# Kernel tuning notes

Hardware: AMD Instinct MI355X
Metric: run time of the kernel (lower is better)

## Reference

```python
import jax, jax.numpy as jnp
import numpy as np

EPS = 1e-6

def _log_g(x):
    # log of continuous g(x) = where(x>=0, x+0.5, sigmoid(x)) from minGRU paper
    return jnp.where(x >= 0, jnp.log(jax.nn.relu(x) + 0.5), -jax.nn.softplus(-x))

def setup_inputs() -> dict:
    key = jax.random.key(0)
    ks = jax.random.split(key, 4)
    B, S, D, E = 4, 2048, 1024, 8
    scale = D ** -0.5
    return {
        "inputs": jax.random.normal(ks[0], (B, S, D), dtype=jnp.float32),
        "norm_weight": jnp.ones((D,), jnp.float32),
        "router_w": jax.random.normal(ks[1], (E, D), jnp.float32) * scale,
        "router_b": jnp.zeros((E,), jnp.float32),
        "w_hg": jax.random.normal(ks[2], (E, 2 * D, D), jnp.float32) * scale,
        "w_out": jax.random.normal(ks[3], (E, D, D), jnp.float32) * scale,
    }

def reference(inputs, norm_weight, router_w, router_b, w_hg, w_out):
    D = inputs.shape[-1]
    # --- RMSNorm ---
    x = inputs * jax.lax.rsqrt(jnp.mean(inputs * inputs, axis=-1, keepdims=True) + EPS) * norm_weight
    # --- SMEAR: per-sample soft merge of expert weights via mean-pooled routing ---
    probs = jax.nn.softmax(jnp.mean(x, axis=1) @ router_w.T + router_b, axis=-1)  # [B,E]
    W_hg = jnp.einsum('be,ekd->bkd', probs, w_hg)    # [B,2D,D] merged to_hidden_and_gate
    W_out = jnp.einsum('be,eod->bod', probs, w_out)  # [B,D,D]  merged to_out
    # --- minGRU with merged weights (log-space parallel scan, no initial state) ---
    hg = jnp.einsum('bsd,bkd->bsk', x, W_hg)         # [B,S,2D]
    hidden, gate = hg[..., :D], hg[..., D:]
    log_coeffs = -jax.nn.softplus(gate)                      # log(1 - z_t)
    log_values = -jax.nn.softplus(-gate) + _log_g(hidden)    # log z_t + log g(h~_t)
    a_star = jnp.cumsum(log_coeffs, axis=1)
    log_h = a_star + jax.lax.cumlogsumexp(log_values - a_star, axis=1)
    h = jnp.exp(log_h)                               # [B,S,D] recurrent states
    new_state = h[:, -1:]                            # [B,1,D]
    out = jnp.einsum('bsk,bok->bso', h, W_out)       # proj_out
    aux_loss = jnp.zeros((), inputs.dtype)
    return (out + inputs, new_state, aux_loss)
```

## Files before the change

### kernel.cpp

```cpp
#include <hip/hip_runtime.h>
#include <hip/hip_bf16.h>
#include <hip/hip_fp16.h>

#define B_  4
#define S_  2048
#define D_  1024
#define E_  8
#define K2_ 2048

#define CHUNKS 64
#define CLEN   32

typedef __attribute__((ext_vector_type(8))) short short8;
typedef __attribute__((ext_vector_type(4))) float floatx4;

__device__ __forceinline__ void gld16(const void* g, const void* l) {
    __builtin_amdgcn_global_load_lds(
        (const __attribute__((address_space(1))) unsigned int*)g,
        (__attribute__((address_space(3))) unsigned int*)l, 16, 0, 0);
}

__device__ __forceinline__ unsigned short f2bf(float f) {
    unsigned int u = __float_as_uint(f);
    u += 0x7fffu + ((u >> 16) & 1u);
    return (unsigned short)(u >> 16);
}

__global__ void rmsnorm_k(const float* __restrict__ in, const float* __restrict__ nw,
                          __hip_bfloat16* __restrict__ x) {
    int b = blockIdx.y, s = blockIdx.x, t = threadIdx.x;
    const float4* row = (const float4*)(in + ((size_t)b * S_ + s) * D_);
    float4 v = row[t];
    float ss = v.x * v.x + v.y * v.y + v.z * v.z + v.w * v.w;
#pragma unroll
    for (int o = 32; o > 0; o >>= 1) ss += __shfl_down(ss, o, 64);
    __shared__ float ls[4];
    if ((t & 63) == 0) ls[t >> 6] = ss;
    __syncthreads();
    float tot = ls[0] + ls[1] + ls[2] + ls[3];
    float rs = rsqrtf(tot * (1.0f / (float)D_) + 1e-6f);
    float4 w = ((const float4*)nw)[t];
    ushort4 o;
    o.x = f2bf(v.x * rs * w.x); o.y = f2bf(v.y * rs * w.y);
    o.z = f2bf(v.z * rs * w.z); o.w = f2bf(v.w * rs * w.w);
    ((ushort4*)(x + ((size_t)b * S_ + s) * D_))[t] = o;
}

__global__ void xsum_k(const __hip_bfloat16* __restrict__ x, float* __restrict__ xs) {
    int d = blockIdx.x * 256 + threadIdx.x;
    int b = blockIdx.y;
    int s0 = blockIdx.z * 128;
    const __hip_bfloat16* p = x + ((size_t)b * S_ + s0) * D_ + d;
    float acc = 0.0f;
#pragma unroll 4
    for (int s = 0; s < 128; s++) { acc += __bfloat162float(*p); p += D_; }
    atomicAdd(&xs[b * D_ + d], acc);
}

__global__ void router_k(const float* __restrict__ xs, const float* __restrict__ rw,
                         const float* __restrict__ rb, float* __restrict__ probs,
                         float* __restrict__ aux) {
    int t = threadIdx.x;
    if (t == 255) *aux = 0.0f;
    int pair = t >> 3, sub = t & 7;
    int b = pair >> 3, e = pair & 7;
    float acc = 0.0f;
#pragma unroll 8
    for (int d = sub; d < D_; d += 8) acc += xs[b * D_ + d] * rw[e * D_ + d];
#pragma unroll
    for (int o = 4; o > 0; o >>= 1) acc += __shfl_down(acc, o, 8);
    __shared__ float lg[32];
    if (sub == 0) lg[pair] = acc * (1.0f / (float)S_) + rb[e];
    __syncthreads();
    if (t < 4) {
        float m = -1e30f;
        for (int e2 = 0; e2 < 8; e2++) m = fmaxf(m, lg[t * 8 + e2]);
        float ssum = 0.0f; float ex[8];
        for (int e2 = 0; e2 < 8; e2++) { ex[e2] = expf(lg[t * 8 + e2] - m); ssum += ex[e2]; }
        for (int e2 = 0; e2 < 8; e2++) probs[t * 8 + e2] = ex[e2] / ssum;
    }
}

__global__ void mix_k(const float* __restrict__ probs, const float* __restrict__ whg_e,
                      const float* __restrict__ wout_e, __hip_bfloat16* __restrict__ Whg,
                      __hip_bfloat16* __restrict__ Wout) {
    __shared__ float P[32];
    int t = threadIdx.x;
    if (t < 32) P[t] = probs[t];
    __syncthreads();
    size_t i4 = (size_t)blockIdx.x * 256 + t;
    const size_t T1q = (size_t)K2_ * D_ / 4;
    const size_t T2q = (size_t)D_ * D_ / 4;
    float4 a0 = {0,0,0,0}, a1 = {0,0,0,0}, a2 = {0,0,0,0}, a3 = {0,0,0,0};
    if (i4 < T1q) {
        const float4* src = (const float4*)whg_e;
#pragma unroll
        for (int e = 0; e < 8; e++) {
            float4 wv = src[(size_t)e * T1q + i4];
            float p0 = P[e], p1 = P[8 + e], p2 = P[16 + e], p3 = P[24 + e];
            a0.x += p0 * wv.x; a0.y += p0 * wv.y; a0.z += p0 * wv.z; a0.w += p0 * wv.w;
            a1.x += p1 * wv.x; a1.y += p1 * wv.y; a1.z += p1 * wv.z; a1.w += p1 * wv.w;
            a2.x += p2 * wv.x; a2.y += p2 * wv.y; a2.z += p2 * wv.z; a2.w += p2 * wv.w;
            a3.x += p3 * wv.x; a3.y += p3 * wv.y; a3.z += p3 * wv.z; a3.w += p3 * wv.w;
        }
        ushort4* dst = (ushort4*)Whg;
        ushort4 o;
        o.x = f2bf(a0.x); o.y = f2bf(a0.y); o.z = f2bf(a0.z); o.w = f2bf(a0.w);
        dst[0 * T1q + i4] = o;
        o.x = f2bf(a1.x); o.y = f2bf(a1.y); o.z = f2bf(a1.z); o.w = f2bf(a1.w);
        dst[1 * T1q + i4] = o;
        o.x = f2bf(a2.x); o.y = f2bf(a2.y); o.z = f2bf(a2.z); o.w = f2bf(a2.w);
        dst[2 * T1q + i4] = o;
        o.x = f2bf(a3.x); o.y = f2bf(a3.y); o.z = f2bf(a3.z); o.w = f2bf(a3.w);
        dst[3 * T1q + i4] = o;
    } else {
        size_t j4 = i4 - T1q;
        const float4* src = (const float4*)wout_e;
#pragma unroll
        for (int e = 0; e < 8; e++) {
            float4 wv = src[(size_t)e * T2q + j4];
            float p0 = P[e], p1 = P[8 + e], p2 = P[16 + e], p3 = P[24 + e];
            a0.x += p0 * wv.x; a0.y += p0 * wv.y; a0.z += p0 * wv.z; a0.w += p0 * wv.w;
            a1.x += p1 * wv.x; a1.y += p1 * wv.y; a1.z += p1 * wv.z; a1.w += p1 * wv.w;
            a2.x += p2 * wv.x; a2.y += p2 * wv.y; a2.z += p2 * wv.z; a2.w += p2 * wv.w;
            a3.x += p3 * wv.x; a3.y += p3 * wv.y; a3.z += p3 * wv.z; a3.w += p3 * wv.w;
        }
        ushort4* dst = (ushort4*)Wout;
        ushort4 o;
        o.x = f2bf(a0.x); o.y = f2bf(a0.y); o.z = f2bf(a0.z); o.w = f2bf(a0.w);
        dst[0 * T2q + j4] = o;
        o.x = f2bf(a1.x); o.y = f2bf(a1.y); o.z = f2bf(a1.z); o.w = f2bf(a1.w);
        dst[1 * T2q + j4] = o;
        o.x = f2bf(a2.x); o.y = f2bf(a2.y); o.z = f2bf(a2.z); o.w = f2bf(a2.w);
        dst[2 * T2q + j4] = o;
        o.x = f2bf(a3.x); o.y = f2bf(a3.y); o.z = f2bf(a3.z); o.w = f2bf(a3.w);
        dst[3 * T2q + j4] = o;
    }
}

__global__ __launch_bounds__(512, 2) void gemm_hg_cv(
    const __hip_bfloat16* __restrict__ A, const __hip_bfloat16* __restrict__ Bm,
    __half2* __restrict__ cv) {
    const int K = D_;
    int bz = blockIdx.z;
    A  += (size_t)bz * S_ * D_;
    Bm += (size_t)bz * K2_ * D_;
    __half2* CV = cv + (size_t)bz * S_ * D_;
    int id = blockIdx.x;
    int sw = (id & 7) * 8 + (id >> 3);
    int m0 = (sw >> 3) * 256, n0 = (sw & 7) * 128;
    __shared__ __hip_bfloat16 lA[2][256][64];
    __shared__ __hip_bfloat16 lBh[2][128][64];
    __shared__ __hip_bfloat16 lBg[2][128][64];
    int t = threadIdx.x;
    int w = t >> 6, lane = t & 63;
    int lm = lane & 15, quad = lane >> 4;
    int wr = w >> 1, wc = w & 1;
    floatx4 acch[4][4] = {};
    floatx4 accg[4][4] = {};
    int srow = lane >> 3;
    int swzb = ((lane & 7) ^ srow) * 16;

    const __hip_bfloat16* Bh = Bm;
    const __hip_bfloat16* Bg = Bm + (size_t)D_ * K;

    const char* pA[4]; const char* pBhp[2]; const char* pBgp[2];
#pragma unroll
    for (int it = 0; it < 4; it++)
        pA[it] = (const char*)(A + (size_t)(m0 + (w * 4 + it) * 8 + srow) * K) + swzb;
#pragma unroll
    for (int it = 0; it < 2; it++) {
        pBhp[it] = (const char*)(Bh + (size_t)(n0 + (w * 2 + it) * 8 + srow) * K) + swzb;
        pBgp[it] = (const char*)(Bg + (size_t)(n0 + (w * 2 + it) * 8 + srow) * K) + swzb;
    }

    auto stage_part = [&](int bb, int part) {
        if (part == 0) {
            gld16(pA[0], &lA[bb][(w * 4 + 0) * 8][0]); pA[0] += 128;
            gld16(pA[1], &lA[bb][(w * 4 + 1) * 8][0]); pA[1] += 128;
            gld16(pBhp[0], &lBh[bb][(w * 2 + 0) * 8][0]); pBhp[0] += 128;
            gld16(pBgp[0], &lBg[bb][(w * 2 + 0) * 8][0]); pBgp[0] += 128;
        } else {
            gld16(pA[2], &lA[bb][(w * 4 + 2) * 8][0]); pA[2] += 128;
            gld16(pA[3], &lA[bb][(w * 4 + 3) * 8][0]); pA[3] += 128;
            gld16(pBhp[1], &lBh[bb][(w * 2 + 1) * 8][0]); pBhp[1] += 128;
            gld16(pBgp[1], &lBg[bb][(w * 2 + 1) * 8][0]); pBgp[1] += 128;
        }
    };

    stage_part(0, 0); stage_part(0, 1);
    int cur = 0;
    for (int kt = 0; kt < 16; kt++) {
        asm volatile("s_waitcnt vmcnt(0)" ::: "memory");
        __builtin_amdgcn_s_barrier();
        bool pre = (kt < 15);
#pragma unroll
        for (int p = 0; p < 4; p++) {
            const int kh = p & 1, bjh = p >> 1;
            const int off = ((kh * 4 + quad) ^ (lm & 7)) * 16;
            short8 af[4], bhf[2], bgf[2];
#pragma unroll
            for (int i = 0; i < 4; i++)
                af[i] = *(const short8*)((const char*)&lA[cur][wr * 64 + i * 16 + lm][0] + off);
#pragma unroll
            for (int jj = 0; jj < 2; jj++) {
                int j = bjh * 2 + jj;
                bhf[jj] = *(const short8*)((const char*)&lBh[cur][wc * 64 + j * 16 + lm][0] + off);
                bgf[jj] = *(const short8*)((const char*)&lBg[cur][wc * 64 + j * 16 + lm][0] + off);
            }
            if (pre && p < 2) stage_part(cur ^ 1, p);
            __builtin_amdgcn_s_barrier();
            asm volatile("s_waitcnt lgkmcnt(0)" ::: "memory");
            __builtin_amdgcn_sched_barrier(0);
            __builtin_amdgcn_s_setprio(1);
#pragma unroll
            for (int i = 0; i < 4; i++)
#pragma unroll
                for (int jj = 0; jj < 2; jj++) {
                    int j = bjh * 2 + jj;
                    acch[i][j] = __builtin_amdgcn_mfma_f32_16x16x32_bf16(
                        af[i], bhf[jj], acch[i][j], 0, 0, 0);
                    accg[i][j] = __builtin_amdgcn_mfma_f32_16x16x32_bf16(
                        af[i], bgf[jj], accg[i][j], 0, 0, 0);
                }
            __builtin_amdgcn_s_setprio(0);
            __builtin_amdgcn_s_barrier();
        }
        cur ^= 1;
    }
#pragma unroll
    for (int i = 0; i < 4; i++) {
#pragma unroll
        for (int j = 0; j < 4; j++) {
#pragma unroll
            for (int r = 0; r < 4; r++) {
                int m = m0 + wr * 64 + i * 16 + quad * 4 + r;
                int n = n0 + wc * 64 + j * 16 + lm;
                float hid = acch[i][j][r];
                float g   = accg[i][j][r];
                float eg  = expf(g);
                float c   = 1.0f / (1.0f + eg);
                float sg  = 1.0f - c;
                float gfn = (hid >= 0.0f) ? (hid + 0.5f)
                                          : (1.0f / (1.0f + expf(-hid)));
                CV[(size_t)m * D_ + n] = __floats2half2_rn(c, sg * gfn);
            }
        }
    }
}

#define TM 128
#define TN 128
#define TBK 64
__global__ __launch_bounds__(256) void gemm_bf16_bt(
    const __hip_bfloat16* __restrict__ A, const __hip_bfloat16* __restrict__ Bm,
    float* __restrict__ C, const float* __restrict__ R,
    int M, int N, int K, size_t sa, size_t sb, size_t sc, size_t sr) {
    int bz = blockIdx.z;
    A += (size_t)bz * sa; Bm += (size_t)bz * sb; C += (size_t)bz * sc;
    if (R) R += (size_t)bz * sr;
    int id = blockIdx.x;
    int sw = (id & 7) * 16 + (id >> 3);
    int m0 = (sw >> 3) * TM, n0 = (sw & 7) * TN;
    __shared__ __hip_bfloat16 lA[2][TM][TBK];
    __shared__ __hip_bfloat16 lB[2][TN][TBK];
    int t = threadIdx.x;
    int w = t >> 6, lane = t & 63;
    int lm = lane & 15, quad = lane >> 4;
    int wr = w >> 1, wc = w & 1;
    floatx4 acc[4][4] = {};
    int srow = lane >> 3;
    int swzb = ((lane & 7) ^ srow) * 16;

    const char* pA[4]; const char* pB[4];
#pragma unroll
    for (int it = 0; it < 4; it++) {
        pA[it] = (const char*)(A + (size_t)(m0 + (w * 4 + it) * 8 + srow) * K) + swzb;
        pB[it] = (const char*)(Bm + (size_t)(n0 + (w * 4 + it) * 8 + srow) * K) + swzb;
    }

    auto stage = [&](int bb) {
#pragma unroll
        for (int it = 0; it < 4; it++) {
            gld16(pA[it], &lA[bb][(w * 4 + it) * 8][0]); pA[it] += 128;
            gld16(pB[it], &lB[bb][(w * 4 + it) * 8][0]); pB[it] += 128;
        }
    };

    stage(0);
    int cur = 0;
    for (int k0 = 0; k0 < K; k0 += TBK) {
        if (k0 + TBK < K) {
            stage(cur ^ 1);
            asm volatile("s_waitcnt vmcnt(8)" ::: "memory");
        } else {
            asm volatile("s_waitcnt vmcnt(0)" ::: "memory");
        }
        __builtin_amdgcn_s_barrier();
#pragma unroll
        for (int kk = 0; kk < TBK; kk += 32) {
            short8 af[4], bf[4];
            int p = (((kk >> 3) + quad) ^ (lm & 7)) * 8;
#pragma unroll
            for (int i = 0; i < 4; i++)
                af[i] = *(const short8*)(&lA[cur][wr * 64 + i * 16 + lm][p]);
#pragma unroll
            for (int j = 0; j < 4; j++)
                bf[j] = *(const short8*)(&lB[cur][wc * 64 + j * 16 + lm][p]);
            __builtin_amdgcn_s_setprio(1);
#pragma unroll
            for (int i = 0; i < 4; i++)
#pragma unroll
                for (int j = 0; j < 4; j++)
                    acc[i][j] = __builtin_amdgcn_mfma_f32_16x16x32_bf16(
                        af[i], bf[j], acc[i][j], 0, 0, 0);
            __builtin_amdgcn_s_setprio(0);
        }
        asm volatile("s_waitcnt lgkmcnt(0)" ::: "memory");
        __builtin_amdgcn_s_barrier();
        cur ^= 1;
    }
#pragma unroll
    for (int i = 0; i < 4; i++) {
#pragma unroll
        for (int j = 0; j < 4; j++) {
#pragma unroll
            for (int r = 0; r < 4; r++) {
                int m = m0 + wr * 64 + i * 16 + quad * 4 + r;
                int n = n0 + wc * 64 + j * 16 + lm;
                float v = acc[i][j][r];
                if (R) v += R[(size_t)m * N + n];
                __builtin_nontemporal_store(v, &C[(size_t)m * N + n]);
            }
        }
    }
}

__global__ void scanA_k(const __half2* __restrict__ cv, float* __restrict__ Cc,
                        float* __restrict__ Vc) {
    int c = blockIdx.x, b = blockIdx.y, t = threadIdx.x;
    const float4* p = (const float4*)(cv + (size_t)(b * S_ + c * CLEN) * D_) + t;
    float P0 = 1, P1 = 1, P2 = 1, P3 = 1;
    float V0 = 0, V1 = 0, V2 = 0, V3 = 0;
#pragma unroll 4
    for (int s = 0; s < CLEN; s++) {
        float4 raw = p[(size_t)s * (D_ / 4)];
        const __half2* e = (const __half2*)&raw;
        float c0 = __low2float(e[0]), v0 = __high2float(e[0]);
        float c1 = __low2float(e[1]), v1 = __high2float(e[1]);
        float c2 = __low2float(e[2]), v2 = __high2float(e[2]);
        float c3 = __low2float(e[3]), v3 = __high2float(e[3]);
        P0 *= c0; V0 = fmaf(c0, V0, v0);
        P1 *= c1; V1 = fmaf(c1, V1, v1);
        P2 *= c2; V2 = fmaf(c2, V2, v2);
        P3 *= c3; V3 = fmaf(c3, V3, v3);
    }
    size_t q = ((size_t)(b * CHUNKS + c)) * (D_ / 4) + t;
    ((float4*)Cc)[q] = make_float4(P0, P1, P2, P3);
    ((float4*)Vc)[q] = make_float4(V0, V1, V2, V3);
}

__global__ void scanC_k(const __half2* __restrict__ cv, const float* __restrict__ Cc,
                        const float* __restrict__ Vc,
                        __hip_bfloat16* __restrict__ hout, float* __restrict__ ns) {
    int c = blockIdx.x, b = blockIdx.y, t = threadIdx.x;
    float h0 = 0, h1 = 0, h2 = 0, h3 = 0;
#pragma unroll 4
    for (int cc = 0; cc < c; cc++) {
        size_t q = ((size_t)(b * CHUNKS + cc)) * (D_ / 4) + t;
        float4 C4 = ((const float4*)Cc)[q];
        float4 V4 = ((const float4*)Vc)[q];
        h0 = fmaf(C4.x, h0, V4.x); h1 = fmaf(C4.y, h1, V4.y);
        h2 = fmaf(C4.z, h2, V4.z); h3 = fmaf(C4.w, h3, V4.w);
    }
    const float4* p = (const float4*)(cv + (size_t)(b * S_ + c * CLEN) * D_) + t;
    ushort4* hq = (ushort4*)(hout + (size_t)(b * S_ + c * CLEN) * D_) + t;
#pragma unroll 4
    for (int s = 0; s < CLEN; s++) {
        float4 raw = p[(size_t)s * (D_ / 4)];
        const __half2* e = (const __half2*)&raw;
        h0 = fmaf(__low2float(e[0]), h0, __high2float(e[0]));
        h1 = fmaf(__low2float(e[1]), h1, __high2float(e[1]));
        h2 = fmaf(__low2float(e[2]), h2, __high2float(e[2]));
        h3 = fmaf(__low2float(e[3]), h3, __high2float(e[3]));
        ushort4 o;
        o.x = f2bf(h0); o.y = f2bf(h1); o.z = f2bf(h2); o.w = f2bf(h3);
        hq[(size_t)s * (D_ / 4)] = o;
    }
    if (c == CHUNKS - 1)
        ((float4*)(ns + (size_t)b * D_))[t] = make_float4(h0, h1, h2, h3);
}

extern "C" void kernel_launch(void* const* d_in, const int* in_sizes, int n_in,
                              void* d_out_v, int out_size, void* d_ws, size_t ws_size,
                              hipStream_t stream) {
    const float* inputs = (const float*)d_in[0];
    const float* nw     = (const float*)d_in[1];
    const float* rw     = (const float*)d_in[2];
    const float* rb     = (const float*)d_in[3];
    const float* whg_e  = (const float*)d_in[4];
    const float* wout_e = (const float*)d_in[5];
    float* out = (float*)d_out_v;

    float* ws = (float*)d_ws;
    __half2*        cv      = (__half2*)ws;
    __hip_bfloat16* x_bf    = (__hip_bfloat16*)(ws + 8388608);
    __hip_bfloat16* h_bf    = (__hip_bfloat16*)(ws + 12582912);
    __hip_bfloat16* Whg_bf  = (__hip_bfloat16*)(ws + 16777216);
    __hip_bfloat16* Wout_bf = (__hip_bfloat16*)(ws + 20971520);
    float* xsum  = ws + 23068672;
    float* probs = ws + 23072768;
    float* Cc    = ws + 23072800;
    float* Vc    = ws + 23334944;

    hipMemsetAsync(xsum, 0, (size_t)B_ * D_ * sizeof(float), stream);

    rmsnorm_k<<<dim3(S_, B_), 256, 0, stream>>>(inputs, nw, x_bf);
    xsum_k<<<dim3(D_ / 256, B_, 16), 256, 0, stream>>>(x_bf, xsum);
    router_k<<<1, 256, 0, stream>>>(xsum, rw, rb, probs,
                                    out + (size_t)B_ * S_ * D_ + (size_t)B_ * D_);
    mix_k<<<3072, 256, 0, stream>>>(probs, whg_e, wout_e, Whg_bf, Wout_bf);

    gemm_hg_cv<<<dim3(64, 1, B_), 512, 0, stream>>>(x_bf, Whg_bf, cv);

    scanA_k<<<dim3(CHUNKS, B_), 256, 0, stream>>>(cv, Cc, Vc);
    scanC_k<<<dim3(CHUNKS, B_), 256, 0, stream>>>(
        cv, Cc, Vc, h_bf, out + (size_t)B_ * S_ * D_);

    gemm_bf16_bt<<<dim3(128, 1, B_), 256, 0, stream>>>(
        h_bf, Wout_bf, out, inputs, S_, D_, D_,
        (size_t)S_ * D_, (size_t)D_ * D_, (size_t)S_ * D_, (size_t)S_ * D_);
}
```

Before: 302.1 us.

## Split GEMM LDS tiles into K-halves with finer-grained staged prefetch

Both GEMM kernels now store each 64-wide K tile as two 32-wide halves with a new 4-chunk XOR swizzle. Each half is prefetched separately, and the wait is vmcnt(4) instead of draining all loads. Fewer barriers are used per K-tile, and the B fragment loads are split so the second set of reads overlaps with MFMA issue. The goal is to hide global-to-LDS latency and cut synchronization stalls, at the cost of more complex waitcnt bookkeeping that is easy to get subtly wrong.

```diff
diff --git a/kernel.cpp b/kernel.cpp
--- a/kernel.cpp
+++ b/kernel.cpp
@@ -149,84 +149,126 @@
     int id = blockIdx.x;
     int sw = (id & 7) * 8 + (id >> 3);
     int m0 = (sw >> 3) * 256, n0 = (sw & 7) * 128;
-    __shared__ __hip_bfloat16 lA[2][256][64];
-    __shared__ __hip_bfloat16 lBh[2][128][64];
-    __shared__ __hip_bfloat16 lBg[2][128][64];
+    __shared__ __hip_bfloat16 lA[2][2][256][32];
+    __shared__ __hip_bfloat16 lBh[2][2][128][32];
+    __shared__ __hip_bfloat16 lBg[2][2][128][32];
     int t = threadIdx.x;
     int w = t >> 6, lane = t & 63;
     int lm = lane & 15, quad = lane >> 4;
     int wr = w >> 1, wc = w & 1;
     floatx4 acch[4][4] = {};
     floatx4 accg[4][4] = {};
-    int srow = lane >> 3;
-    int swzb = ((lane & 7) ^ srow) * 16;
+    int rloc = lane >> 2;
+    int swz4 = ((lane & 3) ^ ((lane >> 3) & 3)) * 16;
+    int pch  = (quad ^ ((lm >> 1) & 3)) * 16;
 
     const __hip_bfloat16* Bh = Bm;
     const __hip_bfloat16* Bg = Bm + (size_t)D_ * K;
 
-    const char* pA[4]; const char* pBhp[2]; const char* pBgp[2];
-#pragma unroll
-    for (int it = 0; it < 4; it++)
-        pA[it] = (const char*)(A + (size_t)(m0 + (w * 4 + it) * 8 + srow) * K) + swzb;
-#pragma unroll
-    for (int it = 0; it < 2; it++) {
-        pBhp[it] = (const char*)(Bh + (size_t)(n0 + (w * 2 + it) * 8 + srow) * K) + swzb;
-        pBgp[it] = (const char*)(Bg + (size_t)(n0 + (w * 2 + it) * 8 + srow) * K) + swzb;
-    }
-
-    auto stage_part = [&](int bb, int part) {
-        if (part == 0) {
-            gld16(pA[0], &lA[bb][(w * 4 + 0) * 8][0]); pA[0] += 128;
-            gld16(pA[1], &lA[bb][(w * 4 + 1) * 8][0]); pA[1] += 128;
-            gld16(pBhp[0], &lBh[bb][(w * 2 + 0) * 8][0]); pBhp[0] += 128;
-            gld16(pBgp[0], &lBg[bb][(w * 2 + 0) * 8][0]); pBgp[0] += 128;
-        } else {
-            gld16(pA[2], &lA[bb][(w * 4 + 2) * 8][0]); pA[2] += 128;
-            gld16(pA[3], &lA[bb][(w * 4 + 3) * 8][0]); pA[3] += 128;
-            gld16(pBhp[1], &lBh[bb][(w * 2 + 1) * 8][0]); pBhp[1] += 128;
-            gld16(pBgp[1], &lBg[bb][(w * 2 + 1) * 8][0]); pBgp[1] += 128;
-        }
+    const char* pA0 = (const char*)(A  + (size_t)(m0 + (w * 2 + 0) * 16 + rloc) * K) + swz4;
+    const char* pA1 = (const char*)(A  + (size_t)(m0 + (w * 2 + 1) * 16 + rloc) * K) + swz4;
+    const char* pBhp = (const char*)(Bh + (size_t)(n0 + w * 16 + rloc) * K) + swz4;
+    const char* pBgp = (const char*)(Bg + (size_t)(n0 + w * 16 + rloc) * K) + swz4;
+
+    auto stage_kh0 = [&](int bb) {
+        gld16(pA0, &lA[bb][0][(w * 2 + 0) * 16][0]);
+        gld16(pA1, &lA[bb][0][(w * 2 + 1) * 16][0]);
+        gld16(pBhp, &lBh[bb][0][w * 16][0]);
+        gld16(pBgp, &lBg[bb][0][w * 16][0]);
     };
-
-    stage_part(0, 0); stage_part(0, 1);
-    int cur = 0;
+    auto stage_kh1 = [&](int bb) {
+        gld16(pA0 + 64, &lA[bb][1][(w * 2 + 0) * 16][0]);
+        gld16(pA1 + 64, &lA[bb][1][(w * 2 + 1) * 16][0]);
+        gld16(pBhp + 64, &lBh[bb][1][w * 16][0]);
+        gld16(pBgp + 64, &lBg[bb][1][w * 16][0]);
+        pA0 += 128; pA1 += 128; pBhp += 128; pBgp += 128;
+    };
+
+    stage_kh0(0); stage_kh1(0);
     for (int kt = 0; kt < 16; kt++) {
-        asm volatile("s_waitcnt vmcnt(0)" ::: "memory");
+        int cur = kt & 1, nxt = cur ^ 1;
+        bool pre = (kt < 15);
+        asm volatile("s_waitcnt vmcnt(4)" ::: "memory");
         __builtin_amdgcn_s_barrier();
-        bool pre = (kt < 15);
-#pragma unroll
-        for (int p = 0; p < 4; p++) {
-            const int kh = p & 1, bjh = p >> 1;
-            const int off = ((kh * 4 + quad) ^ (lm & 7)) * 16;
-            short8 af[4], bhf[2], bgf[2];
-#pragma unroll
-            for (int i = 0; i < 4; i++)
-                af[i] = *(const short8*)((const char*)&lA[cur][wr * 64 + i * 16 + lm][0] + off);
+        short8 af[4], bh0[2], bg0[2];
+#pragma unroll
+        for (int i = 0; i < 4; i++)
+            af[i] = *(const short8*)((const char*)&lA[cur][0][wr * 64 + i * 16 + lm][0] + pch);
+#pragma unroll
+        for (int jj = 0; jj < 2; jj++) {
+            bh0[jj] = *(const short8*)((const char*)&lBh[cur][0][wc * 64 + jj * 16 + lm][0] + pch);
+            bg0[jj] = *(const short8*)((const char*)&lBg[cur][0][wc * 64 + jj * 16 + lm][0] + pch);
+        }
+        if (pre) stage_kh0(nxt);
+        asm volatile("s_waitcnt lgkmcnt(0)" ::: "memory");
+        __builtin_amdgcn_sched_barrier(0);
+        __builtin_amdgcn_s_setprio(1);
+#pragma unroll
+        for (int i = 0; i < 4; i++)
 #pragma unroll
             for (int jj = 0; jj < 2; jj++) {
-                int j = bjh * 2 + jj;
-                bhf[jj] = *(const short8*)((const char*)&lBh[cur][wc * 64 + j * 16 + lm][0] + off);
-                bgf[jj] = *(const short8*)((const char*)&lBg[cur][wc * 64 + j * 16 + lm][0] + off);
+                acch[i][jj] = __builtin_amdgcn_mfma_f32_16x16x32_bf16(af[i], bh0[jj], acch[i][jj], 0, 0, 0);
+                accg[i][jj] = __builtin_amdgcn_mfma_f32_16x16x32_bf16(af[i], bg0[jj], accg[i][jj], 0, 0, 0);
             }
-            if (pre && p < 2) stage_part(cur ^ 1, p);
-            __builtin_amdgcn_s_barrier();
-            asm volatile("s_waitcnt lgkmcnt(0)" ::: "memory");
-            __builtin_amdgcn_sched_barrier(0);
-            __builtin_amdgcn_s_setprio(1);
-#pragma unroll
-            for (int i = 0; i < 4; i++)
-#pragma unroll
-                for (int jj = 0; jj < 2; jj++) {
-                    int j = bjh * 2 + jj;
-                    acch[i][j] = __builtin_amdgcn_mfma_f32_16x16x32_bf16(
-                        af[i], bhf[jj], acch[i][j], 0, 0, 0);
-                    accg[i][j] = __builtin_amdgcn_mfma_f32_16x16x32_bf16(
-                        af[i], bgf[jj], accg[i][j], 0, 0, 0);
-                }
-            __builtin_amdgcn_s_setprio(0);
-            __builtin_amdgcn_s_barrier();
-        }
-        cur ^= 1;
+        __builtin_amdgcn_s_setprio(0);
+        short8 bh1[2], bg1[2];
+#pragma unroll
+        for (int jj = 0; jj < 2; jj++) {
+            bh1[jj] = *(const short8*)((const char*)&lBh[cur][0][wc * 64 + (jj + 2) * 16 + lm][0] + pch);
+            bg1[jj] = *(const short8*)((const char*)&lBg[cur][0][wc * 64 + (jj + 2) * 16 + lm][0] + pch);
+        }
+        asm volatile("s_waitcnt lgkmcnt(0)" ::: "memory");
+        __builtin_amdgcn_sched_barrier(0);
+        __builtin_amdgcn_s_setprio(1);
+#pragma unroll
+        for (int i = 0; i < 4; i++)
+#pragma unroll
+            for (int jj = 0; jj < 2; jj++) {
+                acch[i][jj + 2] = __builtin_amdgcn_mfma_f32_16x16x32_bf16(af[i], bh1[jj], acch[i][jj + 2], 0, 0, 0);
+                accg[i][jj + 2] = __builtin_amdgcn_mfma_f32_16x16x32_bf16(af[i], bg1[jj], accg[i][jj + 2], 0, 0, 0);
+            }
+        __builtin_amdgcn_s_setprio(0);
+        if (pre) asm volatile("s_waitcnt vmcnt(4)" ::: "memory");
+        else     asm volatile("s_waitcnt vmcnt(0)" ::: "memory");
+        __builtin_amdgcn_s_barrier();
+        short8 a1f[4], bh2[2], bg2[2];
+#pragma unroll
+        for (int i = 0; i < 4; i++)
+            a1f[i] = *(const short8*)((const char*)&lA[cur][1][wr * 64 + i * 16 + lm][0] + pch);
+#pragma unroll
+        for (int jj = 0; jj < 2; jj++) {
+            bh2[jj] = *(const short8*)((const char*)&lBh[cur][1][wc * 64 + jj * 16 + lm][0] + pch);
+            bg2[jj] = *(const short8*)((const char*)&lBg[cur][1][wc * 64 + jj * 16 + lm][0] + pch);
+        }
+        if (pre) stage_kh1(nxt);
+        asm volatile("s_waitcnt lgkmcnt(0)" ::: "memory");
+        __builtin_amdgcn_sched_barrier(0);
+        __builtin_amdgcn_s_setprio(1);
+#pragma unroll
+        for (int i = 0; i < 4; i++)
+#pragma unroll
+            for (int jj = 0; jj < 2; jj++) {
+                acch[i][jj] = __builtin_amdgcn_mfma_f32_16x16x32_bf16(a1f[i], bh2[jj], acch[i][jj], 0, 0, 0);
+                accg[i][jj] = __builtin_amdgcn_mfma_f32_16x16x32_bf16(a1f[i], bg2[jj], accg[i][jj], 0, 0, 0);
+            }
+        __builtin_amdgcn_s_setprio(0);
+        short8 bh3[2], bg3[2];
+#pragma unroll
+        for (int jj = 0; jj < 2; jj++) {
+            bh3[jj] = *(const short8*)((const char*)&lBh[cur][1][wc * 64 + (jj + 2) * 16 + lm][0] + pch);
+            bg3[jj] = *(const short8*)((const char*)&lBg[cur][1][wc * 64 + (jj + 2) * 16 + lm][0] + pch);
+        }
+        asm volatile("s_waitcnt lgkmcnt(0)" ::: "memory");
+        __builtin_amdgcn_sched_barrier(0);
+        __builtin_amdgcn_s_setprio(1);
+#pragma unroll
+        for (int i = 0; i < 4; i++)
+#pragma unroll
+            for (int jj = 0; jj < 2; jj++) {
+                acch[i][jj + 2] = __builtin_amdgcn_mfma_f32_16x16x32_bf16(a1f[i], bh3[jj], acch[i][jj + 2], 0, 0, 0);
+                accg[i][jj + 2] = __builtin_amdgcn_mfma_f32_16x16x32_bf16(a1f[i], bg3[jj], accg[i][jj + 2], 0, 0, 0);
+            }
+        __builtin_amdgcn_s_setprio(0);
     }
 #pragma unroll
     for (int i = 0; i < 4; i++) {
@@ -249,9 +291,6 @@
     }
 }
 
-#define TM 128
-#define TN 128
-#define TBK 64
 __global__ __launch_bounds__(256) void gemm_bf16_bt(
     const __hip_bfloat16* __restrict__ A, const __hip_bfloat16* __restrict__ Bm,
     float* __restrict__ C, const float* __restrict__ R,
@@ -261,64 +300,107 @@
     if (R) R += (size_t)bz * sr;
     int id = blockIdx.x;
     int sw = (id & 7) * 16 + (id >> 3);
-    int m0 = (sw >> 3) * TM, n0 = (sw & 7) * TN;
-    __shared__ __hip_bfloat16 lA[2][TM][TBK];
-    __shared__ __hip_bfloat16 lB[2][TN][TBK];
+    int m0 = (sw >> 3) * 128, n0 = (sw & 7) * 128;
+    __shared__ __hip_bfloat16 lA[2][2][128][32];
+    __shared__ __hip_bfloat16 lB[2][2][128][32];
     int t = threadIdx.x;
     int w = t >> 6, lane = t & 63;
     int lm = lane & 15, quad = lane >> 4;
     int wr = w >> 1, wc = w & 1;
     floatx4 acc[4][4] = {};
-    int srow = lane >> 3;
-    int swzb = ((lane & 7) ^ srow) * 16;
-
-    const char* pA[4]; const char* pB[4];
-#pragma unroll
-    for (int it = 0; it < 4; it++) {
-        pA[it] = (const char*)(A + (size_t)(m0 + (w * 4 + it) * 8 + srow) * K) + swzb;
-        pB[it] = (const char*)(Bm + (size_t)(n0 + (w * 4 + it) * 8 + srow) * K) + swzb;
-    }
-
-    auto stage = [&](int bb) {
-#pragma unroll
-        for (int it = 0; it < 4; it++) {
-            gld16(pA[it], &lA[bb][(w * 4 + it) * 8][0]); pA[it] += 128;
-            gld16(pB[it], &lB[bb][(w * 4 + it) * 8][0]); pB[it] += 128;
-        }
+    int rloc = lane >> 2;
+    int swz4 = ((lane & 3) ^ ((lane >> 3) & 3)) * 16;
+    int pch  = (quad ^ ((lm >> 1) & 3)) * 16;
+
+    const char* pA0 = (const char*)(A  + (size_t)(m0 + (w * 2 + 0) * 16 + rloc) * K) + swz4;
+    const char* pA1 = (const char*)(A  + (size_t)(m0 + (w * 2 + 1) * 16 + rloc) * K) + swz4;
+    const char* pB0 = (const char*)(Bm + (size_t)(n0 + (w * 2 + 0) * 16 + rloc) * K) + swz4;
+    const char* pB1 = (const char*)(Bm + (size_t)(n0 + (w * 2 + 1) * 16 + rloc) * K) + swz4;
+
+    auto stage_kh0 = [&](int bb) {
+        gld16(pA0, &lA[bb][0][(w * 2 + 0) * 16][0]);
+        gld16(pA1, &lA[bb][0][(w * 2 + 1) * 16][0]);
+        gld16(pB0, &lB[bb][0][(w * 2 + 0) * 16][0]);
+        gld16(pB1, &lB[bb][0][(w * 2 + 1) * 16][0]);
     };
-
-    stage(0);
-    int cur = 0;
-    for (int k0 = 0; k0 < K; k0 += TBK) {
-        if (k0 + TBK < K) {
-            stage(cur ^ 1);
-            asm volatile("s_waitcnt vmcnt(8)" ::: "memory");
-        } else {
-            asm volatile("s_waitcnt vmcnt(0)" ::: "memory");
-        }
+    auto stage_kh1 = [&](int bb) {
+        gld16(pA0 + 64, &lA[bb][1][(w * 2 + 0) * 16][0]);
+        gld16(pA1 + 64, &lA[bb][1][(w * 2 + 1) * 16][0]);
+        gld16(pB0 + 64, &lB[bb][1][(w * 2 + 0) * 16][0]);
+        gld16(pB1 + 64, &lB[bb][1][(w * 2 + 1) * 16][0]);
+        pA0 += 128; pA1 += 128; pB0 += 128; pB1 += 128;
+    };
+
+    stage_kh0(0); stage_kh1(0);
+    int NT = K / 64;
+    for (int kt = 0; kt < NT; kt++) {
+        int cur = kt & 1, nxt = cur ^ 1;
+        bool pre = (kt < NT - 1);
+        asm volatile("s_waitcnt vmcnt(4)" ::: "memory");
         __builtin_amdgcn_s_barrier();
-#pragma unroll
-        for (int kk = 0; kk < TBK; kk += 32) {
-            short8 af[4], bf[4];
-            int p = (((kk >> 3) + quad) ^ (lm & 7)) * 8;
-#pragma unroll
-            for (int i = 0; i < 4; i++)
-                af[i] = *(const short8*)(&lA[cur][wr * 64 + i * 16 + lm][p]);
-#pragma unroll
-            for (int j = 0; j < 4; j++)
-                bf[j] = *(const short8*)(&lB[cur][wc * 64 + j * 16 + lm][p]);
-            __builtin_amdgcn_s_setprio(1);
-#pragma unroll
-            for (int i = 0; i < 4; i++)
-#pragma unroll
-                for (int j = 0; j < 4; j++)
-                    acc[i][j] = __builtin_amdgcn_mfma_f32_16x16x32_bf16(
-                        af[i], bf[j], acc[i][j], 0, 0, 0);
-            __builtin_amdgcn_s_setprio(0);
-        }
-        asm volatile("s_waitcnt lgkmcnt(0)" ::: "memory");
+        short8 af[4], bf0[2];
+#pragma unroll
+        for (int i = 0; i < 4; i++)
+            af[i] = *(const short8*)((const char*)&lA[cur][0][wr * 64 + i * 16 + lm][0] + pch);
+#pragma unroll
+        for (int jj = 0; jj < 2; jj++)
+            bf0[jj] = *(const short8*)((const char*)&lB[cur][0][wc * 64 + jj * 16 + lm][0] + pch);
+        if (pre) stage_kh0(nxt);
+        asm volatile("s_waitcnt lgkmcnt(0)" ::: "memory");
+        __builtin_amdgcn_sched_barrier(0);
+        __builtin_amdgcn_s_setprio(1);
+#pragma unroll
+        for (int i = 0; i < 4; i++)
+#pragma unroll
+            for (int jj = 0; jj < 2; jj++)
+                acc[i][jj] = __builtin_amdgcn_mfma_f32_16x16x32_bf16(af[i], bf0[jj], acc[i][jj], 0, 0, 0);
+        __builtin_amdgcn_s_setprio(0);
+        short8 bf1[2];
+#pragma unroll
+        for (int jj = 0; jj < 2; jj++)
+            bf1[jj] = *(const short8*)((const char*)&lB[cur][0][wc * 64 + (jj + 2) * 16 + lm][0] + pch);
+        asm volatile("s_waitcnt lgkmcnt(0)" ::: "memory");
+        __builtin_amdgcn_sched_barrier(0);
+        __builtin_amdgcn_s_setprio(1);
+#pragma unroll
+        for (int i = 0; i < 4; i++)
+#pragma unroll
+            for (int jj = 0; jj < 2; jj++)
+                acc[i][jj + 2] = __builtin_amdgcn_mfma_f32_16x16x32_bf16(af[i], bf1[jj], acc[i][jj + 2], 0, 0, 0);
+        __builtin_amdgcn_s_setprio(0);
+        if (pre) asm volatile("s_waitcnt vmcnt(4)" ::: "memory");
+        else     asm volatile("s_waitcnt vmcnt(0)" ::: "memory");
         __builtin_amdgcn_s_barrier();
-        cur ^= 1;
+        short8 a1f[4], bf2[2];
+#pragma unroll
+        for (int i = 0; i < 4; i++)
+            a1f[i] = *(const short8*)((const char*)&lA[cur][1][wr * 64 + i * 16 + lm][0] + pch);
+#pragma unroll
+        for (int jj = 0; jj < 2; jj++)
+            bf2[jj] = *(const short8*)((const char*)&lB[cur][1][wc * 64 + jj * 16 + lm][0] + pch);
+        if (pre) stage_kh1(nxt);
+        asm volatile("s_waitcnt lgkmcnt(0)" ::: "memory");
+        __builtin_amdgcn_sched_barrier(0);
+        __builtin_amdgcn_s_setprio(1);
+#pragma unroll
+        for (int i = 0; i < 4; i++)
+#pragma unroll
+            for (int jj = 0; jj < 2; jj++)
+                acc[i][jj] = __builtin_amdgcn_mfma_f32_16x16x32_bf16(a1f[i], bf2[jj], acc[i][jj], 0, 0, 0);
+        __builtin_amdgcn_s_setprio(0);
+        short8 bf3[2];
+#pragma unroll
+        for (int jj = 0; jj < 2; jj++)
+            bf3[jj] = *(const short8*)((const char*)&lB[cur][1][wc * 64 + (jj + 2) * 16 + lm][0] + pch);
+        asm volatile("s_waitcnt lgkmcnt(0)" ::: "memory");
+        __builtin_amdgcn_sched_barrier(0);
+        __builtin_amdgcn_s_setprio(1);
+#pragma unroll
+        for (int i = 0; i < 4; i++)
+#pragma unroll
+            for (int jj = 0; jj < 2; jj++)
+                acc[i][jj + 2] = __builtin_amdgcn_mfma_f32_16x16x32_bf16(a1f[i], bf3[jj], acc[i][jj + 2], 0, 0, 0);
+        __builtin_amdgcn_s_setprio(0);
     }
 #pragma unroll
     for (int i = 0; i < 4; i++) {
```

After: 304.4 us. Within noise of the previous version (+0.8%).
